# Performance work log

Measured on AMD Instinct MI355X. Metric: run time of the kernel, lower is better.

Reference implementation:

```python
import jax, jax.numpy as jnp
import numpy as np

N = 33554432  # 2**25 elements, 128 MB fp32

def setup_inputs() -> dict:
    key = jax.random.key(0)
    x = jax.random.normal(key, (N,), dtype=jnp.float32)
    return {"x": x}

def reference(x) -> jnp.ndarray:
    # Numerically-stable (safe) softmax over the flat vector:
    # m = max(x); y = exp(x - m) / sum(exp(x - m))
    return jax.nn.softmax(x, axis=-1)
```

## Files before the change

### kernel.cpp

```cpp
#include <hip/hip_runtime.h>
#include <math.h>

#define NBLK 2048
#define NTHR 256

typedef float f32x4 __attribute__((ext_vector_type(4)));

__device__ __forceinline__ void ms_combine(float& m, float& s, float m2, float s2) {
    float mn = fmaxf(m, m2);
    s = s * __expf(m - mn) + s2 * __expf(m2 - mn);
    m = mn;
}

__global__ __launch_bounds__(NTHR) void softmax_partials(
        const float* __restrict__ x, long n4, float* __restrict__ ws) {
    const f32x4* __restrict__ x4 = (const f32x4*)x;
    long tid    = (long)blockIdx.x * blockDim.x + threadIdx.x;
    long stride = (long)gridDim.x * blockDim.x;

    float m = -INFINITY, s = 0.0f;
    for (long i = tid; i < n4; i += stride) {
        f32x4 v = x4[i];
        float vm = fmaxf(fmaxf(v.x, v.y), fmaxf(v.z, v.w));
        if (vm > m) { s *= __expf(m - vm); m = vm; }
        s += __expf(v.x - m) + __expf(v.y - m)
           + __expf(v.z - m) + __expf(v.w - m);
    }

    #pragma unroll
    for (int off = 32; off > 0; off >>= 1) {
        float m2 = __shfl_down(m, off);
        float s2 = __shfl_down(s, off);
        ms_combine(m, s, m2, s2);
    }

    __shared__ float sm[NTHR / 64], ss[NTHR / 64];
    int wid = threadIdx.x >> 6;
    if ((threadIdx.x & 63) == 0) { sm[wid] = m; ss[wid] = s; }
    __syncthreads();
    if (threadIdx.x == 0) {
        m = sm[0]; s = ss[0];
        #pragma unroll
        for (int w = 1; w < NTHR / 64; ++w) ms_combine(m, s, sm[w], ss[w]);
        ws[blockIdx.x]             = m;
        ws[gridDim.x + blockIdx.x] = s;
    }
}

__global__ __launch_bounds__(NTHR) void softmax_write(
        const float* __restrict__ x, float* __restrict__ out, long n4,
        const float* __restrict__ ws, int nparts) {
    float m = -INFINITY, s = 0.0f;
    for (int i = threadIdx.x; i < nparts; i += NTHR) {
        ms_combine(m, s, ws[i], ws[nparts + i]);
    }
    #pragma unroll
    for (int off = 32; off > 0; off >>= 1) {
        float m2 = __shfl_down(m, off);
        float s2 = __shfl_down(s, off);
        ms_combine(m, s, m2, s2);
    }
    __shared__ float sm[NTHR / 64], ss[NTHR / 64];
    __shared__ float g[2];
    int wid = threadIdx.x >> 6;
    if ((threadIdx.x & 63) == 0) { sm[wid] = m; ss[wid] = s; }
    __syncthreads();
    if (threadIdx.x == 0) {
        m = sm[0]; s = ss[0];
        #pragma unroll
        for (int w = 1; w < NTHR / 64; ++w) ms_combine(m, s, sm[w], ss[w]);
        g[0] = m;
        g[1] = 1.0f / s;
    }
    __syncthreads();
    const float gm   = g[0];
    const float ginv = g[1];

    const f32x4* __restrict__ x4 = (const f32x4*)x;
    f32x4* __restrict__ o4 = (f32x4*)out;
    long tid    = (long)blockIdx.x * blockDim.x + threadIdx.x;
    long stride = (long)gridDim.x * blockDim.x;
    for (long i = tid; i < n4; i += stride) {
        f32x4 v = x4[i];
        f32x4 o;
        o.x = __expf(v.x - gm) * ginv;
        o.y = __expf(v.y - gm) * ginv;
        o.z = __expf(v.z - gm) * ginv;
        o.w = __expf(v.w - gm) * ginv;
        __builtin_nontemporal_store(o, &o4[i]);
    }
}

extern "C" void kernel_launch(void* const* d_in, const int* in_sizes, int n_in,
                              void* d_out, int out_size, void* d_ws, size_t ws_size,
                              hipStream_t stream) {
    const float* x = (const float*)d_in[0];
    float* out     = (float*)d_out;
    float* ws      = (float*)d_ws;
    long n  = (long)in_sizes[0];
    long n4 = n >> 2;

    softmax_partials<<<NBLK, NTHR, 0, stream>>>(x, n4, ws);
    softmax_write<<<NBLK, NTHR, 0, stream>>>(x, out, n4, ws, NBLK);
}
```

Measured before the change: 70.19 us.

## Fuse softmax passes into cooperative kernel caching input in registers

Replaces the two-kernel softmax with a single cooperative kernel that loads most of each thread's input slice into registers, computes local max and sum, synchronises the whole grid, then writes outputs from the register copy. The remaining elements beyond the register capacity are streamed twice as before. The aim is to avoid rereading most of the input from memory and to drop a kernel launch, at the cost of heavy register use, low occupancy, and a grid-wide barrier. Falls back to the original two-kernel path if the cooperative launch fails.

```diff
diff --git a/kernel.cpp b/kernel.cpp
--- a/kernel.cpp
+++ b/kernel.cpp
@@ -1,8 +1,14 @@
 #include <hip/hip_runtime.h>
+#include <hip/hip_cooperative_groups.h>
 #include <math.h>
 
+namespace cg = cooperative_groups;
+
+#define CBLK 512
+#define NTHR 256
+#define REGN 44
+
 #define NBLK 2048
-#define NTHR 256
 
 typedef float f32x4 __attribute__((ext_vector_type(4)));
 
@@ -12,12 +18,101 @@
     m = mn;
 }
 
+__device__ __forceinline__ void block_reduce_broadcast(float& m, float& s) {
+    #pragma unroll
+    for (int off = 32; off > 0; off >>= 1) {
+        float m2 = __shfl_down(m, off);
+        float s2 = __shfl_down(s, off);
+        ms_combine(m, s, m2, s2);
+    }
+    __shared__ float sm[NTHR / 64], ss[NTHR / 64], g[2];
+    int wid = threadIdx.x >> 6;
+    if ((threadIdx.x & 63) == 0) { sm[wid] = m; ss[wid] = s; }
+    __syncthreads();
+    if (threadIdx.x == 0) {
+        m = sm[0]; s = ss[0];
+        #pragma unroll
+        for (int w = 1; w < NTHR / 64; ++w) ms_combine(m, s, sm[w], ss[w]);
+        g[0] = m; g[1] = s;
+    }
+    __syncthreads();
+    m = g[0]; s = g[1];
+    __syncthreads();
+}
+
+__global__ __launch_bounds__(NTHR, 2) void softmax_coop(
+        const float* __restrict__ x, float* __restrict__ out,
+        float* __restrict__ ws, long n4) {
+    const f32x4* __restrict__ x4 = (const f32x4*)x;
+    f32x4* __restrict__ o4 = (f32x4*)out;
+    const long T = (long)CBLK * NTHR;
+    const long t = (long)blockIdx.x * NTHR + threadIdx.x;
+
+    f32x4 v[REGN];
+    #pragma unroll
+    for (int j = 0; j < REGN; ++j) v[j] = x4[t + (long)j * T];
+
+    float m = -INFINITY;
+    #pragma unroll
+    for (int j = 0; j < REGN; ++j)
+        m = fmaxf(m, fmaxf(fmaxf(v[j].x, v[j].y), fmaxf(v[j].z, v[j].w)));
+
+    float mt = -INFINITY, st = 0.0f;
+    for (long i = (long)REGN * T + t; i < n4; i += T) {
+        f32x4 w = x4[i];
+        float vm = fmaxf(fmaxf(w.x, w.y), fmaxf(w.z, w.w));
+        if (vm > mt) { st *= __expf(mt - vm); mt = vm; }
+        st += __expf(w.x - mt) + __expf(w.y - mt)
+            + __expf(w.z - mt) + __expf(w.w - mt);
+    }
+
+    float mf = fmaxf(m, mt);
+    float s = 0.0f;
+    #pragma unroll
+    for (int j = 0; j < REGN; ++j)
+        s += __expf(v[j].x - mf) + __expf(v[j].y - mf)
+           + __expf(v[j].z - mf) + __expf(v[j].w - mf);
+    s += st * __expf(mt - mf);
+
+    block_reduce_broadcast(mf, s);
+    if (threadIdx.x == 0) {
+        ws[blockIdx.x]        = mf;
+        ws[CBLK + blockIdx.x] = s;
+    }
+    __threadfence();
+    cg::this_grid().sync();
+
+    float gm = -INFINITY, gs = 0.0f;
+    for (int i = threadIdx.x; i < CBLK; i += NTHR)
+        ms_combine(gm, gs, ws[i], ws[CBLK + i]);
+    block_reduce_broadcast(gm, gs);
+    const float ginv = 1.0f / gs;
+
+    #pragma unroll
+    for (int j = 0; j < REGN; ++j) {
+        f32x4 o;
+        o.x = __expf(v[j].x - gm) * ginv;
+        o.y = __expf(v[j].y - gm) * ginv;
+        o.z = __expf(v[j].z - gm) * ginv;
+        o.w = __expf(v[j].w - gm) * ginv;
+        __builtin_nontemporal_store(o, &o4[t + (long)j * T]);
+    }
+    for (long i = (long)REGN * T + t; i < n4; i += T) {
+        f32x4 w = x4[i];
+        f32x4 o;
+        o.x = __expf(w.x - gm) * ginv;
+        o.y = __expf(w.y - gm) * ginv;
+        o.z = __expf(w.z - gm) * ginv;
+        o.w = __expf(w.w - gm) * ginv;
+        __builtin_nontemporal_store(o, &o4[i]);
+    }
+}
+
 __global__ __launch_bounds__(NTHR) void softmax_partials(
         const float* __restrict__ x, long n4, float* __restrict__ ws) {
     const f32x4* __restrict__ x4 = (const f32x4*)x;
     long tid    = (long)blockIdx.x * blockDim.x + threadIdx.x;
     long stride = (long)gridDim.x * blockDim.x;
-
     float m = -INFINITY, s = 0.0f;
     for (long i = tid; i < n4; i += stride) {
         f32x4 v = x4[i];
@@ -26,22 +121,8 @@
         s += __expf(v.x - m) + __expf(v.y - m)
            + __expf(v.z - m) + __expf(v.w - m);
     }
-
-    #pragma unroll
-    for (int off = 32; off > 0; off >>= 1) {
-        float m2 = __shfl_down(m, off);
-        float s2 = __shfl_down(s, off);
-        ms_combine(m, s, m2, s2);
-    }
-
-    __shared__ float sm[NTHR / 64], ss[NTHR / 64];
-    int wid = threadIdx.x >> 6;
-    if ((threadIdx.x & 63) == 0) { sm[wid] = m; ss[wid] = s; }
-    __syncthreads();
+    block_reduce_broadcast(m, s);
     if (threadIdx.x == 0) {
-        m = sm[0]; s = ss[0];
-        #pragma unroll
-        for (int w = 1; w < NTHR / 64; ++w) ms_combine(m, s, sm[w], ss[w]);
         ws[blockIdx.x]             = m;
         ws[gridDim.x + blockIdx.x] = s;
     }
@@ -51,30 +132,10 @@
         const float* __restrict__ x, float* __restrict__ out, long n4,
         const float* __restrict__ ws, int nparts) {
     float m = -INFINITY, s = 0.0f;
-    for (int i = threadIdx.x; i < nparts; i += NTHR) {
+    for (int i = threadIdx.x; i < nparts; i += NTHR)
         ms_combine(m, s, ws[i], ws[nparts + i]);
-    }
-    #pragma unroll
-    for (int off = 32; off > 0; off >>= 1) {
-        float m2 = __shfl_down(m, off);
-        float s2 = __shfl_down(s, off);
-        ms_combine(m, s, m2, s2);
-    }
-    __shared__ float sm[NTHR / 64], ss[NTHR / 64];
-    __shared__ float g[2];
-    int wid = threadIdx.x >> 6;
-    if ((threadIdx.x & 63) == 0) { sm[wid] = m; ss[wid] = s; }
-    __syncthreads();
-    if (threadIdx.x == 0) {
-        m = sm[0]; s = ss[0];
-        #pragma unroll
-        for (int w = 1; w < NTHR / 64; ++w) ms_combine(m, s, sm[w], ss[w]);
-        g[0] = m;
-        g[1] = 1.0f / s;
-    }
-    __syncthreads();
-    const float gm   = g[0];
-    const float ginv = g[1];
+    block_reduce_broadcast(m, s);
+    const float gm = m, ginv = 1.0f / s;
 
     const f32x4* __restrict__ x4 = (const f32x4*)x;
     f32x4* __restrict__ o4 = (f32x4*)out;
@@ -100,6 +161,16 @@
     long n  = (long)in_sizes[0];
     long n4 = n >> 2;
 
-    softmax_partials<<<NBLK, NTHR, 0, stream>>>(x, n4, ws);
-    softmax_write<<<NBLK, NTHR, 0, stream>>>(x, out, n4, ws, NBLK);
+    bool coop_ok = false;
+    if ((n & 3) == 0 && n4 >= (long)REGN * CBLK * NTHR) {
+        void* args[] = { (void*)&x, (void*)&out, (void*)&ws, (void*)&n4 };
+        hipError_t e = hipLaunchCooperativeKernel((const void*)softmax_coop,
+                                                  dim3(CBLK), dim3(NTHR),
+                                                  args, 0, stream);
+        coop_ok = (e == hipSuccess);
+    }
+    if (!coop_ok) {
+        softmax_partials<<<NBLK, NTHR, 0, stream>>>(x, n4, ws);
+        softmax_write<<<NBLK, NTHR, 0, stream>>>(x, out, n4, ws, NBLK);
+    }
 }
```

Result: slower. 148.1 us (+110.9%).
